# Performance work log

Measured on AMD Instinct MI355X. Metric: run time of the kernel, lower is better.

The kernel has to match this reference:

```python
import jax, jax.numpy as jnp
import numpy as np

B = 4096          # events per batch
K = 32            # neighbors stored per node
F = 64            # feat_dim = time_dim = e_feat_dim
H = 128           # hidden_dim = e_feat_dim + time_dim
DIN = 2 * F       # GRU input: [edge_emb | time_emb]
N_NODES = 500_000
N_EDGES = 1_000_000


def setup_inputs() -> dict:
    key = jax.random.key(0)
    ks = jax.random.split(key, 20)
    inp = {}
    inp["src_ids"] = jax.random.randint(ks[0], (B,), 0, N_NODES)
    inp["tgt_ids"] = jax.random.randint(ks[1], (B,), 0, N_NODES)
    inp["bad_ids"] = jax.random.randint(ks[2], (B,), 0, N_NODES)
    inp["cut_time"] = jax.random.uniform(ks[3], (B,)) * 1e4 + 1e4
    inp["ngh_id"] = jax.random.randint(ks[4], (3 * B, K), 0, N_NODES)
    inp["e_idx"] = jax.random.randint(ks[5], (3 * B, K), 0, N_EDGES)
    inp["ngh_ts"] = jax.random.uniform(ks[6], (3 * B, K)) * 1e4
    inp["hidden_store"] = jax.random.normal(ks[7], (3 * B, K, H)) * 0.1
    # frozen raw feature tables (padding row 0 zeroed like padding_idx=0)
    n_feat = jax.random.normal(ks[8], (N_NODES, F)) * 0.1
    inp["n_feat"] = n_feat.at[0].set(0.0)
    e_feat = jax.random.normal(ks[9], (N_EDGES, F)) * 0.1
    inp["e_feat"] = e_feat.at[0].set(0.0)
    # TimeEncode params
    inp["basis_freq"] = jnp.asarray(1.0 / 10 ** np.linspace(0, 9, F), jnp.float32)
    inp["phase"] = jnp.zeros((F,), jnp.float32)
    # GRUCell params (torch layout: [3H, in], gate order r,z,n)
    s = 1.0 / np.sqrt(H)
    inp["W_ih"] = jax.random.uniform(ks[10], (3 * H, DIN), minval=-s, maxval=s)
    inp["W_hh"] = jax.random.uniform(ks[11], (3 * H, H), minval=-s, maxval=s)
    inp["b_ih"] = jax.random.uniform(ks[12], (3 * H,), minval=-s, maxval=s)
    inp["b_hh"] = jax.random.uniform(ks[13], (3 * H,), minval=-s, maxval=s)
    # readout projection (stand-in for GAT output to feat_dim)
    inp["W_out"] = jax.random.normal(ks[14], (F, F + H)) * (1.0 / np.sqrt(F + H))
    inp["b_out"] = jnp.zeros((F,), jnp.float32)
    # MergeLayer (non_linear=True): fc1 [F, 2F], fc2 [1, F]
    inp["fc1_w"] = jax.random.normal(ks[15], (F, 2 * F)) * (1.0 / np.sqrt(2 * F))
    inp["fc1_b"] = jnp.zeros((F,), jnp.float32)
    inp["fc2_w"] = jax.random.normal(ks[16], (1, F)) * (1.0 / np.sqrt(F))
    inp["fc2_b"] = jnp.zeros((1,), jnp.float32)
    return inp


def _gru_cell(x, h, W_ih, W_hh, b_ih, b_hh):
    gx = x @ W_ih.T + b_ih          # [N, 3H]
    gh = h @ W_hh.T + b_hh
    xr, xz, xn = jnp.split(gx, 3, axis=-1)
    hr, hz, hn = jnp.split(gh, 3, axis=-1)
    r = jax.nn.sigmoid(xr + hr)
    z = jax.nn.sigmoid(xz + hz)
    n = jnp.tanh(xn + r * hn)
    return (1.0 - z) * n + z * h


def reference(src_ids, tgt_ids, bad_ids, cut_time, ngh_id, e_idx, ngh_ts,
              hidden_store, n_feat, e_feat, basis_freq, phase,
              W_ih, W_hh, b_ih, b_hh, W_out, b_out,
              fc1_w, fc1_b, fc2_w, fc2_b):
    ids = jnp.concatenate([src_ids, tgt_ids, bad_ids], 0)      # [3B]
    node_raw = n_feat[ids]                                     # [3B, F] gather
    e_emb = e_feat[e_idx]                                      # [3B, K, F] gather
    # cosine time encoding of time delta since neighbor event
    ct = jnp.tile(cut_time, 3)                                 # [3B]
    dt = ct[:, None] - ngh_ts                                  # [3B, K]
    ts_emb = jnp.cos(dt[..., None] * basis_freq + phase)       # [3B, K, F]
    # one GRUCell step per stored neighbor
    x = jnp.concatenate([e_emb, ts_emb], -1).reshape(-1, DIN)  # [3B*K, 2F]
    h = hidden_store.reshape(-1, H)
    h_new = _gru_cell(x, h, W_ih, W_hh, b_ih, b_hh).reshape(3 * B, K, H)
    # masked mean over valid neighbors (ngh_id 0 = padding)
    mask = (ngh_id != 0).astype(h_new.dtype)[..., None]        # [3B, K, 1]
    agg = (h_new * mask).sum(1) / jnp.maximum(mask.sum(1), 1.0)  # [3B, H]
    # readout to feat_dim
    emb = jax.nn.relu(jnp.concatenate([node_raw, agg], -1) @ W_out.T + b_out)
    src_e, tgt_e, bad_e = emb[:B], emb[B:2 * B], emb[2 * B:]
    def merge(x1, x2):
        hcat = jax.nn.relu(jnp.concatenate([x1, x2], -1) @ fc1_w.T + fc1_b)
        return hcat @ fc2_w.T + fc2_b                          # [B, 1]
    pos = merge(src_e, tgt_e)
    neg = merge(src_e, bad_e)
    return jnp.concatenate([pos, neg], -1)                     # [B, 2]
```

## Files before the change

kernel.cpp:

```cpp
#include <hip/hip_runtime.h>
#include <hip/hip_bf16.h>

#define B_SZ   4096

typedef short bf16x8 __attribute__((ext_vector_type(8)));
typedef float f32x4  __attribute__((ext_vector_type(4)));

__device__ __forceinline__ short f2bf(float f) {
    __hip_bfloat16 h = __float2bfloat16(f);
    return *reinterpret_cast<short*>(&h);
}
__device__ __forceinline__ float bf2f(unsigned int u16) {
    unsigned int x = u16 << 16;
    float f;
    __builtin_memcpy(&f, &x, 4);
    return f;
}
__device__ __forceinline__ float fsig(float x) {
    return __builtin_amdgcn_rcpf(1.0f + __expf(-x));
}
__device__ __forceinline__ float ftanhf(float x) {
    return 1.0f - 2.0f * __builtin_amdgcn_rcpf(__expf(2.0f * x) + 1.0f);
}
__device__ __forceinline__ int swz(int row, int cbyte) {
    return row * 512 + (cbyte ^ ((row & 7) << 4));
}

__global__ void prep_kernel(const float* __restrict__ wih, const float* __restrict__ whh,
                            short* __restrict__ wfrag) {
    int idx = blockIdx.x * 256 + threadIdx.x;
    int i   = idx & 7;
    int kh  = (idx >> 3) & 3;
    int j   = (idx >> 5) & 127;
    int gks = idx >> 12;
    int g   = gks >> 3, ks = gks & 7;
    int k   = ks * 32 + kh * 8 + i;
    int r   = g * 128 + j;
    float v = (k < 128) ? wih[r * 128 + k] : whh[r * 128 + (k - 128)];
    wfrag[idx] = f2bf(v);
}

__global__ __launch_bounds__(512, 4) void gru_agg_kernel(
    const int*   __restrict__ ngh_id,
    const int*   __restrict__ e_idx,
    const float* __restrict__ ngh_ts,
    const float* __restrict__ hidden_store,
    const float* __restrict__ e_feat,
    const float* __restrict__ basis_freq,
    const float* __restrict__ phase,
    const float* __restrict__ cut_time,
    const short* __restrict__ wfrag,
    const float* __restrict__ b_ih,
    const float* __restrict__ b_hh,
    float*       __restrict__ agg)
{
    __shared__ __align__(16) char sT[64 * 512];
    __shared__ float sMask[64];
    __shared__ float sInv[2];

    const int bid  = blockIdx.x;
    const int tid  = threadIdx.x;
    const int lane = tid & 63;
    const int wv   = tid >> 6;

    if (wv < 2) {
        const int row  = lane;
        const int flat = bid * 64 + row;
        const int e    = e_idx[flat];
        const float4* src = reinterpret_cast<const float4*>(e_feat + (size_t)e * 64 + wv * 32);
        float v[32];
        #pragma unroll
        for (int t = 0; t < 8; ++t) *reinterpret_cast<float4*>(&v[t * 4]) = src[t];
        union { bf16x8 w[4]; short s[32]; } u;
        #pragma unroll
        for (int i = 0; i < 32; ++i) u.s[i] = f2bf(v[i]);
        const int cb = wv * 64;
        #pragma unroll
        for (int t = 0; t < 4; ++t)
            *reinterpret_cast<bf16x8*>(&sT[swz(row, cb + t * 16)]) = u.w[t];
    } else if (wv < 4) {
        const int row  = lane;
        const int flat = bid * 64 + row;
        if (wv == 2) {
            const int nid = ngh_id[flat];
            sMask[row] = (nid != 0) ? 1.0f : 0.0f;
            unsigned long long mb = __ballot(nid != 0);
            if (lane == 0) {
                int c0n = __popcll(mb & 0xFFFFFFFFull);
                int c1n = __popcll(mb >> 32);
                sInv[0] = 1.0f / (float)(c0n > 1 ? c0n : 1);
                sInv[1] = 1.0f / (float)(c1n > 1 ? c1n : 1);
            }
        }
        const int rnode = bid * 2 + (row >> 5);
        const float dt  = cut_time[rnode & (B_SZ - 1)] - ngh_ts[flat];
        const int f0 = (wv - 2) * 32;
        float v[32];
        #pragma unroll
        for (int i = 0; i < 32; ++i)
            v[i] = __cosf(dt * basis_freq[f0 + i] + phase[f0 + i]);
        union { bf16x8 w[4]; short s[32]; } u;
        #pragma unroll
        for (int i = 0; i < 32; ++i) u.s[i] = f2bf(v[i]);
        const int cb = 128 + f0 * 2;
        #pragma unroll
        for (int t = 0; t < 4; ++t)
            *reinterpret_cast<bf16x8*>(&sT[swz(row, cb + t * 16)]) = u.w[t];
    } else {
        const int hw   = wv - 4;
        const int row  = hw * 16 + (lane >> 2);
        const int flat = bid * 64 + row;
        const int c0   = (lane & 3) * 32;
        const float4* src = reinterpret_cast<const float4*>(hidden_store + (size_t)flat * 128 + c0);
        float v[32];
        #pragma unroll
        for (int t = 0; t < 8; ++t) *reinterpret_cast<float4*>(&v[t * 4]) = src[t];
        union { bf16x8 w[4]; short s[32]; } u;
        #pragma unroll
        for (int i = 0; i < 32; ++i) u.s[i] = f2bf(v[i]);
        const int cb = 256 + c0 * 2;
        #pragma unroll
        for (int t = 0; t < 4; ++t)
            *reinterpret_cast<bf16x8*>(&sT[swz(row, cb + t * 16)]) = u.w[t];
    }
    __syncthreads();

    const int l15 = lane & 15;
    const int kh  = lane >> 4;
    const int jc  = (wv << 4) + l15;

    f32x4 ar[4], az[4], axn[4], ahn[4];
    #pragma unroll
    for (int mf = 0; mf < 4; ++mf) {
        ar[mf]  = (f32x4){0.f, 0.f, 0.f, 0.f};
        az[mf]  = (f32x4){0.f, 0.f, 0.f, 0.f};
        axn[mf] = (f32x4){0.f, 0.f, 0.f, 0.f};
        ahn[mf] = (f32x4){0.f, 0.f, 0.f, 0.f};
    }

    #pragma unroll
    for (int ks = 0; ks < 8; ++ks) {
        bf16x8 a[4];
        #pragma unroll
        for (int mf = 0; mf < 4; ++mf)
            a[mf] = *reinterpret_cast<const bf16x8*>(&sT[swz(mf * 16 + l15, ks * 64 + kh * 16)]);
        bf16x8 br = *reinterpret_cast<const bf16x8*>(wfrag + (((((0 * 8 + ks) * 128 + jc) << 2) + kh) << 3));
        bf16x8 bz = *reinterpret_cast<const bf16x8*>(wfrag + (((((1 * 8 + ks) * 128 + jc) << 2) + kh) << 3));
        bf16x8 bn = *reinterpret_cast<const bf16x8*>(wfrag + (((((2 * 8 + ks) * 128 + jc) << 2) + kh) << 3));
        #pragma unroll
        for (int mf = 0; mf < 4; ++mf)
            ar[mf] = __builtin_amdgcn_mfma_f32_16x16x32_bf16(a[mf], br, ar[mf], 0, 0, 0);
        #pragma unroll
        for (int mf = 0; mf < 4; ++mf)
            az[mf] = __builtin_amdgcn_mfma_f32_16x16x32_bf16(a[mf], bz, az[mf], 0, 0, 0);
        if (ks < 4) {
            #pragma unroll
            for (int mf = 0; mf < 4; ++mf)
                axn[mf] = __builtin_amdgcn_mfma_f32_16x16x32_bf16(a[mf], bn, axn[mf], 0, 0, 0);
        } else {
            #pragma unroll
            for (int mf = 0; mf < 4; ++mf)
                ahn[mf] = __builtin_amdgcn_mfma_f32_16x16x32_bf16(a[mf], bn, ahn[mf], 0, 0, 0);
        }
    }

    const float brz = b_ih[jc] + b_hh[jc];
    const float bzz = b_ih[128 + jc] + b_hh[128 + jc];
    const float bin = b_ih[256 + jc];
    const float bhn = b_hh[256 + jc];

    float s0 = 0.f, s1 = 0.f;
    #pragma unroll
    for (int mf = 0; mf < 4; ++mf) {
        #pragma unroll
        for (int i = 0; i < 4; ++i) {
            const int row = mf * 16 + kh * 4 + i;
            const float rr = fsig(ar[mf][i] + brz);
            const float zz = fsig(az[mf][i] + bzz);
            const float nn = ftanhf(axn[mf][i] + bin + rr * (ahn[mf][i] + bhn));
            const float hc = bf2f(*reinterpret_cast<const unsigned short*>(&sT[swz(row, 256 + jc * 2)]));
            const float hv = ((1.0f - zz) * nn + zz * hc) * sMask[row];
            if (mf < 2) s0 += hv; else s1 += hv;
        }
    }
    s0 += __shfl_xor(s0, 16, 64);
    s0 += __shfl_xor(s0, 32, 64);
    s1 += __shfl_xor(s1, 16, 64);
    s1 += __shfl_xor(s1, 32, 64);
    if (lane < 16) {
        agg[(bid * 2 + 0) * 128 + jc] = s0 * sInv[0];
        agg[(bid * 2 + 1) * 128 + jc] = s1 * sInv[1];
    }
}

__global__ __launch_bounds__(256) void emb_kernel(
    const int*   __restrict__ src_ids, const int* __restrict__ tgt_ids,
    const int*   __restrict__ bad_ids, const float* __restrict__ n_feat,
    const float* __restrict__ W_out,   const float* __restrict__ b_out,
    const float* __restrict__ agg,     float* __restrict__ emb)
{
    __shared__ float sv[16][192];
    const int base = blockIdx.x * 16;
    const int j  = threadIdx.x & 63;
    const int ng = threadIdx.x >> 6;
    #pragma unroll
    for (int n0 = 0; n0 < 4; ++n0) {
        const int n = ng * 4 + n0;
        const int node = base + n;
        int id;
        if (node < B_SZ)          id = src_ids[node];
        else if (node < 2 * B_SZ) id = tgt_ids[node - B_SZ];
        else                      id = bad_ids[node - 2 * B_SZ];
        sv[n][j]       = n_feat[(size_t)id * 64 + j];
        sv[n][64 + j]  = agg[(size_t)node * 128 + j];
        sv[n][128 + j] = agg[(size_t)node * 128 + 64 + j];
    }
    __syncthreads();
    float acc[4];
    const float bj = b_out[j];
    #pragma unroll
    for (int n0 = 0; n0 < 4; ++n0) acc[n0] = bj;
    const float4* wr = reinterpret_cast<const float4*>(W_out + j * 192);
    #pragma unroll 4
    for (int c = 0; c < 48; ++c) {
        float4 w = wr[c];
        #pragma unroll
        for (int n0 = 0; n0 < 4; ++n0) {
            const float* s = &sv[ng * 4 + n0][c * 4];
            acc[n0] += w.x * s[0] + w.y * s[1] + w.z * s[2] + w.w * s[3];
        }
    }
    #pragma unroll
    for (int n0 = 0; n0 < 4; ++n0)
        emb[(size_t)(base + ng * 4 + n0) * 64 + j] = fmaxf(acc[n0], 0.0f);
}

__global__ __launch_bounds__(256) void merge_kernel(
    const float* __restrict__ emb,  const float* __restrict__ fc1_w,
    const float* __restrict__ fc1_b, const float* __restrict__ fc2_w,
    const float* __restrict__ fc2_b, float* __restrict__ out)
{
    __shared__ float se[16][192];
    const int base = blockIdx.x * 16;
    const int j  = threadIdx.x & 63;
    const int ng = threadIdx.x >> 6;
    #pragma unroll
    for (int p0 = 0; p0 < 4; ++p0) {
        const int p = ng * 4 + p0;
        const int i = base + p;
        se[p][j]       = emb[(size_t)i * 64 + j];
        se[p][64 + j]  = emb[(size_t)(B_SZ + i) * 64 + j];
        se[p][128 + j] = emb[(size_t)(2 * B_SZ + i) * 64 + j];
    }
    __syncthreads();
    const float4* w1 = reinterpret_cast<const float4*>(fc1_w + j * 128);
    float sp[4] = {0, 0, 0, 0}, tp[4] = {0, 0, 0, 0}, bp[4] = {0, 0, 0, 0};
    #pragma unroll 4
    for (int c = 0; c < 16; ++c) {
        float4 wa = w1[c];
        float4 wb = w1[16 + c];
        #pragma unroll
        for (int p0 = 0; p0 < 4; ++p0) {
            const float* s = se[ng * 4 + p0];
            const float* sa = &s[c * 4];
            sp[p0] += wa.x * sa[0] + wa.y * sa[1] + wa.z * sa[2] + wa.w * sa[3];
            const float* st = &s[64 + c * 4];
            tp[p0] += wb.x * st[0] + wb.y * st[1] + wb.z * st[2] + wb.w * st[3];
            const float* sb = &s[128 + c * 4];
            bp[p0] += wb.x * sb[0] + wb.y * sb[1] + wb.z * sb[2] + wb.w * sb[3];
        }
    }
    const float b1 = fc1_b[j];
    const float w2 = fc2_w[j];
    #pragma unroll
    for (int p0 = 0; p0 < 4; ++p0) {
        float p = fmaxf(b1 + sp[p0] + tp[p0], 0.f) * w2;
        float n = fmaxf(b1 + sp[p0] + bp[p0], 0.f) * w2;
        #pragma unroll
        for (int m = 32; m >= 1; m >>= 1) {
            p += __shfl_xor(p, m, 64);
            n += __shfl_xor(n, m, 64);
        }
        if (j == 0) {
            const int i = base + ng * 4 + p0;
            out[2 * i]     = p + fc2_b[0];
            out[2 * i + 1] = n + fc2_b[0];
        }
    }
}

extern "C" void kernel_launch(void* const* d_in, const int* in_sizes, int n_in,
                              void* d_out, int out_size, void* d_ws, size_t ws_size,
                              hipStream_t stream) {
    const int*   src_ids  = (const int*)  d_in[0];
    const int*   tgt_ids  = (const int*)  d_in[1];
    const int*   bad_ids  = (const int*)  d_in[2];
    const float* cut_time = (const float*)d_in[3];
    const int*   ngh_id   = (const int*)  d_in[4];
    const int*   e_idx    = (const int*)  d_in[5];
    const float* ngh_ts   = (const float*)d_in[6];
    const float* hidden   = (const float*)d_in[7];
    const float* n_feat   = (const float*)d_in[8];
    const float* e_feat   = (const float*)d_in[9];
    const float* basis    = (const float*)d_in[10];
    const float* phase    = (const float*)d_in[11];
    const float* W_ih     = (const float*)d_in[12];
    const float* W_hh     = (const float*)d_in[13];
    const float* b_ih     = (const float*)d_in[14];
    const float* b_hh     = (const float*)d_in[15];
    const float* W_out    = (const float*)d_in[16];
    const float* b_out    = (const float*)d_in[17];
    const float* fc1_w    = (const float*)d_in[18];
    const float* fc1_b    = (const float*)d_in[19];
    const float* fc2_w    = (const float*)d_in[20];
    const float* fc2_b    = (const float*)d_in[21];

    char* ws = (char*)d_ws;
    short* wfrag = (short*)(ws);
    float* agg   = (float*)(ws + 196608);
    float* emb   = (float*)(ws + 196608 + 6291456);
    float* out   = (float*)d_out;

    hipLaunchKernelGGL(prep_kernel, dim3(384), dim3(256), 0, stream, W_ih, W_hh, wfrag);
    hipLaunchKernelGGL(gru_agg_kernel, dim3(6144), dim3(512), 0, stream,
                       ngh_id, e_idx, ngh_ts, hidden, e_feat, basis, phase, cut_time,
                       wfrag, b_ih, b_hh, agg);
    hipLaunchKernelGGL(emb_kernel, dim3(768), dim3(256), 0, stream,
                       src_ids, tgt_ids, bad_ids, n_feat, W_out, b_out, agg, emb);
    hipLaunchKernelGGL(merge_kernel, dim3(256), dim3(256), 0, stream,
                       emb, fc1_w, fc1_b, fc2_w, fc2_b, out);
}
```

Measured before the change: 181.7 us.

## Process one node per GRU block to halve tile size and raise occupancy

```diff
diff --git a/kernel.cpp b/kernel.cpp
--- a/kernel.cpp
+++ b/kernel.cpp
@@ -24,6 +24,13 @@
 }
 __device__ __forceinline__ int swz(int row, int cbyte) {
     return row * 512 + (cbyte ^ ((row & 7) << 4));
+}
+__device__ __forceinline__ void pack16(const float* v, bf16x8* out) {
+    union { short s[16]; bf16x8 w[2]; } u;
+    #pragma unroll
+    for (int i = 0; i < 16; ++i) u.s[i] = f2bf(v[i]);
+    out[0] = u.w[0];
+    out[1] = u.w[1];
 }
 
 __global__ void prep_kernel(const float* __restrict__ wih, const float* __restrict__ whh,
@@ -40,7 +47,7 @@
     wfrag[idx] = f2bf(v);
 }
 
-__global__ __launch_bounds__(512, 4) void gru_agg_kernel(
+__global__ __launch_bounds__(512, 6) void gru_agg_kernel(
     const int*   __restrict__ ngh_id,
     const int*   __restrict__ e_idx,
     const float* __restrict__ ngh_ts,
@@ -54,74 +61,56 @@
     const float* __restrict__ b_hh,
     float*       __restrict__ agg)
 {
-    __shared__ __align__(16) char sT[64 * 512];
-    __shared__ float sMask[64];
-    __shared__ float sInv[2];
+    __shared__ __align__(16) char sT[32 * 512];
+    __shared__ float sMask[32];
+    __shared__ float sInv;
 
     const int bid  = blockIdx.x;
     const int tid  = threadIdx.x;
     const int lane = tid & 63;
     const int wv   = tid >> 6;
 
-    if (wv < 2) {
-        const int row  = lane;
-        const int flat = bid * 64 + row;
-        const int e    = e_idx[flat];
-        const float4* src = reinterpret_cast<const float4*>(e_feat + (size_t)e * 64 + wv * 32);
-        float v[32];
-        #pragma unroll
-        for (int t = 0; t < 8; ++t) *reinterpret_cast<float4*>(&v[t * 4]) = src[t];
-        union { bf16x8 w[4]; short s[32]; } u;
-        #pragma unroll
-        for (int i = 0; i < 32; ++i) u.s[i] = f2bf(v[i]);
-        const int cb = wv * 64;
-        #pragma unroll
-        for (int t = 0; t < 4; ++t)
-            *reinterpret_cast<bf16x8*>(&sT[swz(row, cb + t * 16)]) = u.w[t];
-    } else if (wv < 4) {
-        const int row  = lane;
-        const int flat = bid * 64 + row;
-        if (wv == 2) {
-            const int nid = ngh_id[flat];
-            sMask[row] = (nid != 0) ? 1.0f : 0.0f;
-            unsigned long long mb = __ballot(nid != 0);
-            if (lane == 0) {
-                int c0n = __popcll(mb & 0xFFFFFFFFull);
-                int c1n = __popcll(mb >> 32);
-                sInv[0] = 1.0f / (float)(c0n > 1 ? c0n : 1);
-                sInv[1] = 1.0f / (float)(c1n > 1 ? c1n : 1);
+    {
+        const int row  = lane & 31;
+        const int h    = lane >> 5;
+        const int flat = bid * 32 + row;
+        float v[16];
+        int cb;
+
+        if (wv < 2) {
+            if (wv == 0) {
+                const int nid = ngh_id[flat];
+                unsigned long long mb = __ballot(nid != 0);
+                if (lane < 32) sMask[row] = (nid != 0) ? 1.0f : 0.0f;
+                if (lane == 0) {
+                    int c = __popcll(mb & 0xFFFFFFFFull);
+                    sInv = 1.0f / (float)(c > 1 ? c : 1);
+                }
             }
-        }
-        const int rnode = bid * 2 + (row >> 5);
-        const float dt  = cut_time[rnode & (B_SZ - 1)] - ngh_ts[flat];
-        const int f0 = (wv - 2) * 32;
-        float v[32];
-        #pragma unroll
-        for (int i = 0; i < 32; ++i)
-            v[i] = __cosf(dt * basis_freq[f0 + i] + phase[f0 + i]);
-        union { bf16x8 w[4]; short s[32]; } u;
-        #pragma unroll
-        for (int i = 0; i < 32; ++i) u.s[i] = f2bf(v[i]);
-        const int cb = 128 + f0 * 2;
-        #pragma unroll
-        for (int t = 0; t < 4; ++t)
-            *reinterpret_cast<bf16x8*>(&sT[swz(row, cb + t * 16)]) = u.w[t];
-    } else {
-        const int hw   = wv - 4;
-        const int row  = hw * 16 + (lane >> 2);
-        const int flat = bid * 64 + row;
-        const int c0   = (lane & 3) * 32;
-        const float4* src = reinterpret_cast<const float4*>(hidden_store + (size_t)flat * 128 + c0);
-        float v[32];
-        #pragma unroll
-        for (int t = 0; t < 8; ++t) *reinterpret_cast<float4*>(&v[t * 4]) = src[t];
-        union { bf16x8 w[4]; short s[32]; } u;
-        #pragma unroll
-        for (int i = 0; i < 32; ++i) u.s[i] = f2bf(v[i]);
-        const int cb = 256 + c0 * 2;
-        #pragma unroll
-        for (int t = 0; t < 4; ++t)
-            *reinterpret_cast<bf16x8*>(&sT[swz(row, cb + t * 16)]) = u.w[t];
+            const int c0 = wv * 32 + h * 16;
+            const int e  = e_idx[flat];
+            const float4* src = reinterpret_cast<const float4*>(e_feat + (size_t)e * 64 + c0);
+            #pragma unroll
+            for (int t = 0; t < 4; ++t) *reinterpret_cast<float4*>(&v[t * 4]) = src[t];
+            cb = c0 * 2;
+        } else if (wv < 4) {
+            const float dt = cut_time[bid & (B_SZ - 1)] - ngh_ts[flat];
+            const int f0 = (wv - 2) * 32 + h * 16;
+            #pragma unroll
+            for (int i = 0; i < 16; ++i)
+                v[i] = __cosf(dt * basis_freq[f0 + i] + phase[f0 + i]);
+            cb = 128 + f0 * 2;
+        } else {
+            const int c0 = (wv - 4) * 32 + h * 16;
+            const float4* src = reinterpret_cast<const float4*>(hidden_store + (size_t)flat * 128 + c0);
+            #pragma unroll
+            for (int t = 0; t < 4; ++t) *reinterpret_cast<float4*>(&v[t * 4]) = src[t];
+            cb = 256 + c0 * 2;
+        }
+        bf16x8 w[2];
+        pack16(v, w);
+        *reinterpret_cast<bf16x8*>(&sT[swz(row, cb)])      = w[0];
+        *reinterpret_cast<bf16x8*>(&sT[swz(row, cb + 16)]) = w[1];
     }
     __syncthreads();
 
@@ -129,9 +118,9 @@
     const int kh  = lane >> 4;
     const int jc  = (wv << 4) + l15;
 
-    f32x4 ar[4], az[4], axn[4], ahn[4];
-    #pragma unroll
-    for (int mf = 0; mf < 4; ++mf) {
+    f32x4 ar[2], az[2], axn[2], ahn[2];
+    #pragma unroll
+    for (int mf = 0; mf < 2; ++mf) {
         ar[mf]  = (f32x4){0.f, 0.f, 0.f, 0.f};
         az[mf]  = (f32x4){0.f, 0.f, 0.f, 0.f};
         axn[mf] = (f32x4){0.f, 0.f, 0.f, 0.f};
@@ -140,26 +129,26 @@
 
     #pragma unroll
     for (int ks = 0; ks < 8; ++ks) {
-        bf16x8 a[4];
-        #pragma unroll
-        for (int mf = 0; mf < 4; ++mf)
+        bf16x8 a[2];
+        #pragma unroll
+        for (int mf = 0; mf < 2; ++mf)
             a[mf] = *reinterpret_cast<const bf16x8*>(&sT[swz(mf * 16 + l15, ks * 64 + kh * 16)]);
         bf16x8 br = *reinterpret_cast<const bf16x8*>(wfrag + (((((0 * 8 + ks) * 128 + jc) << 2) + kh) << 3));
         bf16x8 bz = *reinterpret_cast<const bf16x8*>(wfrag + (((((1 * 8 + ks) * 128 + jc) << 2) + kh) << 3));
         bf16x8 bn = *reinterpret_cast<const bf16x8*>(wfrag + (((((2 * 8 + ks) * 128 + jc) << 2) + kh) << 3));
         #pragma unroll
-        for (int mf = 0; mf < 4; ++mf)
+        for (int mf = 0; mf < 2; ++mf)
             ar[mf] = __builtin_amdgcn_mfma_f32_16x16x32_bf16(a[mf], br, ar[mf], 0, 0, 0);
         #pragma unroll
-        for (int mf = 0; mf < 4; ++mf)
+        for (int mf = 0; mf < 2; ++mf)
             az[mf] = __builtin_amdgcn_mfma_f32_16x16x32_bf16(a[mf], bz, az[mf], 0, 0, 0);
         if (ks < 4) {
             #pragma unroll
-            for (int mf = 0; mf < 4; ++mf)
+            for (int mf = 0; mf < 2; ++mf)
                 axn[mf] = __builtin_amdgcn_mfma_f32_16x16x32_bf16(a[mf], bn, axn[mf], 0, 0, 0);
         } else {
             #pragma unroll
-            for (int mf = 0; mf < 4; ++mf)
+            for (int mf = 0; mf < 2; ++mf)
                 ahn[mf] = __builtin_amdgcn_mfma_f32_16x16x32_bf16(a[mf], bn, ahn[mf], 0, 0, 0);
         }
     }
@@ -169,9 +158,9 @@
     const float bin = b_ih[256 + jc];
     const float bhn = b_hh[256 + jc];
 
-    float s0 = 0.f, s1 = 0.f;
-    #pragma unroll
-    for (int mf = 0; mf < 4; ++mf) {
+    float s = 0.f;
+    #pragma unroll
+    for (int mf = 0; mf < 2; ++mf) {
         #pragma unroll
         for (int i = 0; i < 4; ++i) {
             const int row = mf * 16 + kh * 4 + i;
@@ -179,18 +168,13 @@
             const float zz = fsig(az[mf][i] + bzz);
             const float nn = ftanhf(axn[mf][i] + bin + rr * (ahn[mf][i] + bhn));
             const float hc = bf2f(*reinterpret_cast<const unsigned short*>(&sT[swz(row, 256 + jc * 2)]));
-            const float hv = ((1.0f - zz) * nn + zz * hc) * sMask[row];
-            if (mf < 2) s0 += hv; else s1 += hv;
-        }
-    }
-    s0 += __shfl_xor(s0, 16, 64);
-    s0 += __shfl_xor(s0, 32, 64);
-    s1 += __shfl_xor(s1, 16, 64);
-    s1 += __shfl_xor(s1, 32, 64);
-    if (lane < 16) {
-        agg[(bid * 2 + 0) * 128 + jc] = s0 * sInv[0];
-        agg[(bid * 2 + 1) * 128 + jc] = s1 * sInv[1];
-    }
+            s += ((1.0f - zz) * nn + zz * hc) * sMask[row];
+        }
+    }
+    s += __shfl_xor(s, 16, 64);
+    s += __shfl_xor(s, 32, 64);
+    if (lane < 16)
+        agg[(size_t)bid * 128 + jc] = s * sInv;
 }
 
 __global__ __launch_bounds__(256) void emb_kernel(
@@ -322,7 +306,7 @@
     float* out   = (float*)d_out;
 
     hipLaunchKernelGGL(prep_kernel, dim3(384), dim3(256), 0, stream, W_ih, W_hh, wfrag);
-    hipLaunchKernelGGL(gru_agg_kernel, dim3(6144), dim3(512), 0, stream,
+    hipLaunchKernelGGL(gru_agg_kernel, dim3(12288), dim3(512), 0, stream,
                        ngh_id, e_idx, ngh_ts, hidden, e_feat, basis, phase, cut_time,
                        wfrag, b_ih, b_hh, agg);
     hipLaunchKernelGGL(emb_kernel, dim3(768), dim3(256), 0, stream,
```

After: 229.3 us. 1.26x slower.

## Split GRU gate MFMA phases and pack r/z gates to bf16 to cut registers

Applied to the files above, without the earlier changes.

```diff
diff --git a/kernel.cpp b/kernel.cpp
--- a/kernel.cpp
+++ b/kernel.cpp
@@ -15,6 +15,11 @@
     float f;
     __builtin_memcpy(&f, &x, 4);
     return f;
+}
+__device__ __forceinline__ unsigned int pk2(float a, float b) {
+    unsigned int lo = (unsigned short)f2bf(a);
+    unsigned int hi = (unsigned short)f2bf(b);
+    return lo | (hi << 16);
 }
 __device__ __forceinline__ float fsig(float x) {
     return __builtin_amdgcn_rcpf(1.0f + __expf(-x));
@@ -40,7 +45,7 @@
     wfrag[idx] = f2bf(v);
 }
 
-__global__ __launch_bounds__(512, 4) void gru_agg_kernel(
+__global__ __launch_bounds__(512, 6) void gru_agg_kernel(
     const int*   __restrict__ ngh_id,
     const int*   __restrict__ e_idx,
     const float* __restrict__ ngh_ts,
@@ -129,15 +134,12 @@
     const int kh  = lane >> 4;
     const int jc  = (wv << 4) + l15;
 
-    f32x4 ar[4], az[4], axn[4], ahn[4];
+    f32x4 ar[4], az[4];
     #pragma unroll
     for (int mf = 0; mf < 4; ++mf) {
-        ar[mf]  = (f32x4){0.f, 0.f, 0.f, 0.f};
-        az[mf]  = (f32x4){0.f, 0.f, 0.f, 0.f};
-        axn[mf] = (f32x4){0.f, 0.f, 0.f, 0.f};
-        ahn[mf] = (f32x4){0.f, 0.f, 0.f, 0.f};
-    }
-
+        ar[mf] = (f32x4){0.f, 0.f, 0.f, 0.f};
+        az[mf] = (f32x4){0.f, 0.f, 0.f, 0.f};
+    }
     #pragma unroll
     for (int ks = 0; ks < 8; ++ks) {
         bf16x8 a[4];
@@ -146,13 +148,43 @@
             a[mf] = *reinterpret_cast<const bf16x8*>(&sT[swz(mf * 16 + l15, ks * 64 + kh * 16)]);
         bf16x8 br = *reinterpret_cast<const bf16x8*>(wfrag + (((((0 * 8 + ks) * 128 + jc) << 2) + kh) << 3));
         bf16x8 bz = *reinterpret_cast<const bf16x8*>(wfrag + (((((1 * 8 + ks) * 128 + jc) << 2) + kh) << 3));
-        bf16x8 bn = *reinterpret_cast<const bf16x8*>(wfrag + (((((2 * 8 + ks) * 128 + jc) << 2) + kh) << 3));
         #pragma unroll
         for (int mf = 0; mf < 4; ++mf)
             ar[mf] = __builtin_amdgcn_mfma_f32_16x16x32_bf16(a[mf], br, ar[mf], 0, 0, 0);
         #pragma unroll
         for (int mf = 0; mf < 4; ++mf)
             az[mf] = __builtin_amdgcn_mfma_f32_16x16x32_bf16(a[mf], bz, az[mf], 0, 0, 0);
+    }
+
+    const float brz = b_ih[jc] + b_hh[jc];
+    const float bzz = b_ih[128 + jc] + b_hh[128 + jc];
+    unsigned int rrpk[8], zzpk[8];
+    #pragma unroll
+    for (int mf = 0; mf < 4; ++mf) {
+        #pragma unroll
+        for (int p = 0; p < 2; ++p) {
+            float r0 = fsig(ar[mf][2 * p]     + brz);
+            float r1 = fsig(ar[mf][2 * p + 1] + brz);
+            float z0 = fsig(az[mf][2 * p]     + bzz);
+            float z1 = fsig(az[mf][2 * p + 1] + bzz);
+            rrpk[mf * 2 + p] = pk2(r0, r1);
+            zzpk[mf * 2 + p] = pk2(z0, z1);
+        }
+    }
+
+    f32x4 axn[4], ahn[4];
+    #pragma unroll
+    for (int mf = 0; mf < 4; ++mf) {
+        axn[mf] = (f32x4){0.f, 0.f, 0.f, 0.f};
+        ahn[mf] = (f32x4){0.f, 0.f, 0.f, 0.f};
+    }
+    #pragma unroll
+    for (int ks = 0; ks < 8; ++ks) {
+        bf16x8 a[4];
+        #pragma unroll
+        for (int mf = 0; mf < 4; ++mf)
+            a[mf] = *reinterpret_cast<const bf16x8*>(&sT[swz(mf * 16 + l15, ks * 64 + kh * 16)]);
+        bf16x8 bn = *reinterpret_cast<const bf16x8*>(wfrag + (((((2 * 8 + ks) * 128 + jc) << 2) + kh) << 3));
         if (ks < 4) {
             #pragma unroll
             for (int mf = 0; mf < 4; ++mf)
@@ -164,8 +196,6 @@
         }
     }
 
-    const float brz = b_ih[jc] + b_hh[jc];
-    const float bzz = b_ih[128 + jc] + b_hh[128 + jc];
     const float bin = b_ih[256 + jc];
     const float bhn = b_hh[256 + jc];
 
@@ -175,11 +205,13 @@
         #pragma unroll
         for (int i = 0; i < 4; ++i) {
             const int row = mf * 16 + kh * 4 + i;
-            const float rr = fsig(ar[mf][i] + brz);
-            const float zz = fsig(az[mf][i] + bzz);
-            const float nn = ftanhf(axn[mf][i] + bin + rr * (ahn[mf][i] + bhn));
-            const float hc = bf2f(*reinterpret_cast<const unsigned short*>(&sT[swz(row, 256 + jc * 2)]));
-            const float hv = ((1.0f - zz) * nn + zz * hc) * sMask[row];
+            unsigned int rp = rrpk[mf * 2 + (i >> 1)];
+            unsigned int zp = zzpk[mf * 2 + (i >> 1)];
+            float rr = bf2f((i & 1) ? (rp >> 16) : (rp & 0xffffu));
+            float zz = bf2f((i & 1) ? (zp >> 16) : (zp & 0xffffu));
+            float nn = ftanhf(axn[mf][i] + bin + rr * (ahn[mf][i] + bhn));
+            float hc = bf2f(*reinterpret_cast<const unsigned short*>(&sT[swz(row, 256 + jc * 2)]));
+            float hv = ((1.0f - zz) * nn + zz * hc) * sMask[row];
             if (mf < 2) s0 += hv; else s1 += hv;
         }
     }
```

Measured after the change: 318.4 us. 1.75x slower.

## Make GRU aggregation kernel persistent with async LDS prefetch of next tile

Applied to the files above, without the earlier changes.

```diff
diff --git a/kernel.cpp b/kernel.cpp
--- a/kernel.cpp
+++ b/kernel.cpp
@@ -2,8 +2,10 @@
 #include <hip/hip_bf16.h>
 
 #define B_SZ   4096
+#define NT     12
 
 typedef short bf16x8 __attribute__((ext_vector_type(8)));
+typedef short bf16x4 __attribute__((ext_vector_type(4)));
 typedef float f32x4  __attribute__((ext_vector_type(4)));
 
 __device__ __forceinline__ short f2bf(float f) {
@@ -24,6 +26,12 @@
 }
 __device__ __forceinline__ int swz(int row, int cbyte) {
     return row * 512 + (cbyte ^ ((row & 7) << 4));
+}
+__device__ __forceinline__ void gld16(const float* g, float* l) {
+    __builtin_amdgcn_global_load_lds(
+        (const __attribute__((address_space(1))) void*)g,
+        (__attribute__((address_space(3))) void*)l,
+        16, 0, 0);
 }
 
 __global__ void prep_kernel(const float* __restrict__ wih, const float* __restrict__ whh,
@@ -54,142 +62,181 @@
     const float* __restrict__ b_hh,
     float*       __restrict__ agg)
 {
-    __shared__ __align__(16) char sT[64 * 512];
-    __shared__ float sMask[64];
-    __shared__ float sInv[2];
-
-    const int bid  = blockIdx.x;
+    __shared__ float sE[4096];
+    __shared__ float sH8[8192];
+    __shared__ __align__(16) char sT[32768];
+
     const int tid  = threadIdx.x;
     const int lane = tid & 63;
     const int wv   = tid >> 6;
-
-    if (wv < 2) {
-        const int row  = lane;
-        const int flat = bid * 64 + row;
-        const int e    = e_idx[flat];
-        const float4* src = reinterpret_cast<const float4*>(e_feat + (size_t)e * 64 + wv * 32);
-        float v[32];
-        #pragma unroll
-        for (int t = 0; t < 8; ++t) *reinterpret_cast<float4*>(&v[t * 4]) = src[t];
-        union { bf16x8 w[4]; short s[32]; } u;
-        #pragma unroll
-        for (int i = 0; i < 32; ++i) u.s[i] = f2bf(v[i]);
-        const int cb = wv * 64;
-        #pragma unroll
-        for (int t = 0; t < 4; ++t)
-            *reinterpret_cast<bf16x8*>(&sT[swz(row, cb + t * 16)]) = u.w[t];
-    } else if (wv < 4) {
-        const int row  = lane;
-        const int flat = bid * 64 + row;
-        if (wv == 2) {
-            const int nid = ngh_id[flat];
-            sMask[row] = (nid != 0) ? 1.0f : 0.0f;
-            unsigned long long mb = __ballot(nid != 0);
-            if (lane == 0) {
-                int c0n = __popcll(mb & 0xFFFFFFFFull);
-                int c1n = __popcll(mb >> 32);
-                sInv[0] = 1.0f / (float)(c0n > 1 ? c0n : 1);
-                sInv[1] = 1.0f / (float)(c1n > 1 ? c1n : 1);
-            }
-        }
-        const int rnode = bid * 2 + (row >> 5);
-        const float dt  = cut_time[rnode & (B_SZ - 1)] - ngh_ts[flat];
-        const int f0 = (wv - 2) * 32;
-        float v[32];
-        #pragma unroll
-        for (int i = 0; i < 32; ++i)
-            v[i] = __cosf(dt * basis_freq[f0 + i] + phase[f0 + i]);
-        union { bf16x8 w[4]; short s[32]; } u;
-        #pragma unroll
-        for (int i = 0; i < 32; ++i) u.s[i] = f2bf(v[i]);
-        const int cb = 128 + f0 * 2;
-        #pragma unroll
-        for (int t = 0; t < 4; ++t)
-            *reinterpret_cast<bf16x8*>(&sT[swz(row, cb + t * 16)]) = u.w[t];
-    } else {
-        const int hw   = wv - 4;
-        const int row  = hw * 16 + (lane >> 2);
-        const int flat = bid * 64 + row;
-        const int c0   = (lane & 3) * 32;
-        const float4* src = reinterpret_cast<const float4*>(hidden_store + (size_t)flat * 128 + c0);
-        float v[32];
-        #pragma unroll
-        for (int t = 0; t < 8; ++t) *reinterpret_cast<float4*>(&v[t * 4]) = src[t];
-        union { bf16x8 w[4]; short s[32]; } u;
-        #pragma unroll
-        for (int i = 0; i < 32; ++i) u.s[i] = f2bf(v[i]);
-        const int cb = 256 + c0 * 2;
-        #pragma unroll
-        for (int t = 0; t < 4; ++t)
-            *reinterpret_cast<bf16x8*>(&sT[swz(row, cb + t * 16)]) = u.w[t];
-    }
-    __syncthreads();
-
-    const int l15 = lane & 15;
-    const int kh  = lane >> 4;
-    const int jc  = (wv << 4) + l15;
-
-    f32x4 ar[4], az[4], axn[4], ahn[4];
-    #pragma unroll
-    for (int mf = 0; mf < 4; ++mf) {
-        ar[mf]  = (f32x4){0.f, 0.f, 0.f, 0.f};
-        az[mf]  = (f32x4){0.f, 0.f, 0.f, 0.f};
-        axn[mf] = (f32x4){0.f, 0.f, 0.f, 0.f};
-        ahn[mf] = (f32x4){0.f, 0.f, 0.f, 0.f};
-    }
-
-    #pragma unroll
-    for (int ks = 0; ks < 8; ++ks) {
-        bf16x8 a[4];
-        #pragma unroll
-        for (int mf = 0; mf < 4; ++mf)
-            a[mf] = *reinterpret_cast<const bf16x8*>(&sT[swz(mf * 16 + l15, ks * 64 + kh * 16)]);
-        bf16x8 br = *reinterpret_cast<const bf16x8*>(wfrag + (((((0 * 8 + ks) * 128 + jc) << 2) + kh) << 3));
-        bf16x8 bz = *reinterpret_cast<const bf16x8*>(wfrag + (((((1 * 8 + ks) * 128 + jc) << 2) + kh) << 3));
-        bf16x8 bn = *reinterpret_cast<const bf16x8*>(wfrag + (((((2 * 8 + ks) * 128 + jc) << 2) + kh) << 3));
-        #pragma unroll
-        for (int mf = 0; mf < 4; ++mf)
-            ar[mf] = __builtin_amdgcn_mfma_f32_16x16x32_bf16(a[mf], br, ar[mf], 0, 0, 0);
-        #pragma unroll
-        for (int mf = 0; mf < 4; ++mf)
-            az[mf] = __builtin_amdgcn_mfma_f32_16x16x32_bf16(a[mf], bz, az[mf], 0, 0, 0);
-        if (ks < 4) {
-            #pragma unroll
-            for (int mf = 0; mf < 4; ++mf)
-                axn[mf] = __builtin_amdgcn_mfma_f32_16x16x32_bf16(a[mf], bn, axn[mf], 0, 0, 0);
-        } else {
-            #pragma unroll
-            for (int mf = 0; mf < 4; ++mf)
-                ahn[mf] = __builtin_amdgcn_mfma_f32_16x16x32_bf16(a[mf], bn, ahn[mf], 0, 0, 0);
-        }
-    }
+    const int l15  = lane & 15;
+    const int kh   = lane >> 4;
+    const int jc   = (wv << 4) + l15;
+
+    const int tsrow = tid >> 3;
+    const int tscol = (tid & 7) * 8;
 
     const float brz = b_ih[jc] + b_hh[jc];
     const float bzz = b_ih[128 + jc] + b_hh[128 + jc];
     const float bin = b_ih[256 + jc];
     const float bhn = b_hh[256 + jc];
 
-    float s0 = 0.f, s1 = 0.f;
-    #pragma unroll
-    for (int mf = 0; mf < 4; ++mf) {
-        #pragma unroll
-        for (int i = 0; i < 4; ++i) {
-            const int row = mf * 16 + kh * 4 + i;
-            const float rr = fsig(ar[mf][i] + brz);
-            const float zz = fsig(az[mf][i] + bzz);
-            const float nn = ftanhf(axn[mf][i] + bin + rr * (ahn[mf][i] + bhn));
-            const float hc = bf2f(*reinterpret_cast<const unsigned short*>(&sT[swz(row, 256 + jc * 2)]));
-            const float hv = ((1.0f - zz) * nn + zz * hc) * sMask[row];
-            if (mf < 2) s0 += hv; else s1 += hv;
-        }
-    }
-    s0 += __shfl_xor(s0, 16, 64);
-    s0 += __shfl_xor(s0, 32, 64);
-    s1 += __shfl_xor(s1, 16, 64);
-    s1 += __shfl_xor(s1, 32, 64);
-    if (lane < 16) {
-        agg[(bid * 2 + 0) * 128 + jc] = s0 * sInv[0];
-        agg[(bid * 2 + 1) * 128 + jc] = s1 * sInv[1];
+    const int tile0 = blockIdx.x * NT;
+    const int erow  = wv * 8 + (lane >> 4);
+
+    float tsr  = ngh_ts[(size_t)tile0 * 64 + tsrow];
+    float ctr  = cut_time[(tile0 * 2 + (tsrow >> 5)) & (B_SZ - 1)];
+    int   ngid = ngh_id[(size_t)tile0 * 64 + lane];
+    int iA = e_idx[(size_t)tile0 * 64 + erow];
+    int iB = e_idx[(size_t)tile0 * 64 + erow + 4];
+    gld16(e_feat + (size_t)iA * 64 + l15 * 4, &sE[(wv * 2 + 0) * 256]);
+    gld16(e_feat + (size_t)iB * 64 + l15 * 4, &sE[(wv * 2 + 1) * 256]);
+    #pragma unroll
+    for (int k = 0; k < 4; ++k)
+        gld16(hidden_store + (size_t)(tile0 * 64 + wv * 8 + k * 2 + (lane >> 5)) * 128 + (lane & 31) * 4,
+              &sH8[(wv * 4 + k) * 256]);
+    int cA = e_idx[(size_t)(tile0 + 1) * 64 + erow];
+    int cB = e_idx[(size_t)(tile0 + 1) * 64 + erow + 4];
+
+    __syncthreads();
+
+    {
+        #pragma unroll
+        for (int j = 0; j < 2; ++j) {
+            float4 v = *reinterpret_cast<const float4*>(&sE[(wv * 2 + j) * 256 + lane * 4]);
+            int row = wv * 8 + j * 4 + (lane >> 4);
+            bf16x4 o = { f2bf(v.x), f2bf(v.y), f2bf(v.z), f2bf(v.w) };
+            *reinterpret_cast<bf16x4*>(&sT[swz(row, l15 * 8)]) = o;
+        }
+        #pragma unroll
+        for (int k = 0; k < 4; ++k) {
+            float4 v = *reinterpret_cast<const float4*>(&sH8[(wv * 4 + k) * 256 + lane * 4]);
+            int row = wv * 8 + k * 2 + (lane >> 5);
+            bf16x4 o = { f2bf(v.x), f2bf(v.y), f2bf(v.z), f2bf(v.w) };
+            *reinterpret_cast<bf16x4*>(&sT[swz(row, 256 + (lane & 31) * 8)]) = o;
+        }
+        const float dt = ctr - tsr;
+        union { short s[8]; bf16x8 w; } u;
+        #pragma unroll
+        for (int i = 0; i < 8; ++i)
+            u.s[i] = f2bf(__cosf(dt * basis_freq[tscol + i] + phase[tscol + i]));
+        *reinterpret_cast<bf16x8*>(&sT[swz(tsrow, 128 + (tid & 7) * 16)]) = u.w;
+    }
+    unsigned long long mb = __ballot(ngid != 0);
+    int c0n = __popcll(mb & 0xFFFFFFFFull);
+    int c1n = __popcll(mb >> 32);
+    float inv0 = 1.0f / (float)(c0n > 1 ? c0n : 1);
+    float inv1 = 1.0f / (float)(c1n > 1 ? c1n : 1);
+    __syncthreads();
+
+    #pragma unroll 1
+    for (int t = 0; t < NT; ++t) {
+        const int tt = tile0 + t;
+        float n_tsr = 0.f, n_ctr = 0.f;
+        int   n_ngid = 0;
+        if (t + 1 < NT) {
+            gld16(e_feat + (size_t)cA * 64 + l15 * 4, &sE[(wv * 2 + 0) * 256]);
+            gld16(e_feat + (size_t)cB * 64 + l15 * 4, &sE[(wv * 2 + 1) * 256]);
+            #pragma unroll
+            for (int k = 0; k < 4; ++k)
+                gld16(hidden_store + (size_t)((tt + 1) * 64 + wv * 8 + k * 2 + (lane >> 5)) * 128 + (lane & 31) * 4,
+                      &sH8[(wv * 4 + k) * 256]);
+            n_tsr  = ngh_ts[(size_t)(tt + 1) * 64 + tsrow];
+            n_ctr  = cut_time[((tt + 1) * 2 + (tsrow >> 5)) & (B_SZ - 1)];
+            n_ngid = ngh_id[(size_t)(tt + 1) * 64 + lane];
+            const int t2 = (t + 2 < NT) ? (tt + 2) : (tile0 + NT - 1);
+            cA = e_idx[(size_t)t2 * 64 + erow];
+            cB = e_idx[(size_t)t2 * 64 + erow + 4];
+        }
+
+        f32x4 ar[4], az[4], axn[4], ahn[4];
+        #pragma unroll
+        for (int mf = 0; mf < 4; ++mf) {
+            ar[mf]  = (f32x4){0.f, 0.f, 0.f, 0.f};
+            az[mf]  = (f32x4){0.f, 0.f, 0.f, 0.f};
+            axn[mf] = (f32x4){0.f, 0.f, 0.f, 0.f};
+            ahn[mf] = (f32x4){0.f, 0.f, 0.f, 0.f};
+        }
+        #pragma unroll
+        for (int ks = 0; ks < 8; ++ks) {
+            bf16x8 a[4];
+            #pragma unroll
+            for (int mf = 0; mf < 4; ++mf)
+                a[mf] = *reinterpret_cast<const bf16x8*>(&sT[swz(mf * 16 + l15, ks * 64 + kh * 16)]);
+            bf16x8 br = *reinterpret_cast<const bf16x8*>(wfrag + (((((0 * 8 + ks) * 128 + jc) << 2) + kh) << 3));
+            bf16x8 bz = *reinterpret_cast<const bf16x8*>(wfrag + (((((1 * 8 + ks) * 128 + jc) << 2) + kh) << 3));
+            bf16x8 bn = *reinterpret_cast<const bf16x8*>(wfrag + (((((2 * 8 + ks) * 128 + jc) << 2) + kh) << 3));
+            #pragma unroll
+            for (int mf = 0; mf < 4; ++mf)
+                ar[mf] = __builtin_amdgcn_mfma_f32_16x16x32_bf16(a[mf], br, ar[mf], 0, 0, 0);
+            #pragma unroll
+            for (int mf = 0; mf < 4; ++mf)
+                az[mf] = __builtin_amdgcn_mfma_f32_16x16x32_bf16(a[mf], bz, az[mf], 0, 0, 0);
+            if (ks < 4) {
+                #pragma unroll
+                for (int mf = 0; mf < 4; ++mf)
+                    axn[mf] = __builtin_amdgcn_mfma_f32_16x16x32_bf16(a[mf], bn, axn[mf], 0, 0, 0);
+            } else {
+                #pragma unroll
+                for (int mf = 0; mf < 4; ++mf)
+                    ahn[mf] = __builtin_amdgcn_mfma_f32_16x16x32_bf16(a[mf], bn, ahn[mf], 0, 0, 0);
+            }
+        }
+
+        float s0 = 0.f, s1 = 0.f;
+        #pragma unroll
+        for (int mf = 0; mf < 4; ++mf) {
+            #pragma unroll
+            for (int i = 0; i < 4; ++i) {
+                const int row = mf * 16 + kh * 4 + i;
+                const float rr = fsig(ar[mf][i] + brz);
+                const float zz = fsig(az[mf][i] + bzz);
+                const float nn = ftanhf(axn[mf][i] + bin + rr * (ahn[mf][i] + bhn));
+                const float hc = bf2f(*reinterpret_cast<const unsigned short*>(&sT[swz(row, 256 + jc * 2)]));
+                const float m  = (float)((mb >> row) & 1ull);
+                const float hv = ((1.0f - zz) * nn + zz * hc) * m;
+                if (mf < 2) s0 += hv; else s1 += hv;
+            }
+        }
+        s0 += __shfl_xor(s0, 16, 64);
+        s0 += __shfl_xor(s0, 32, 64);
+        s1 += __shfl_xor(s1, 16, 64);
+        s1 += __shfl_xor(s1, 32, 64);
+        if (lane < 16) {
+            agg[(size_t)(tt * 2 + 0) * 128 + jc] = s0 * inv0;
+            agg[(size_t)(tt * 2 + 1) * 128 + jc] = s1 * inv1;
+        }
+
+        if (t + 1 < NT) {
+            __syncthreads();
+            #pragma unroll
+            for (int j = 0; j < 2; ++j) {
+                float4 v = *reinterpret_cast<const float4*>(&sE[(wv * 2 + j) * 256 + lane * 4]);
+                int row = wv * 8 + j * 4 + (lane >> 4);
+                bf16x4 o = { f2bf(v.x), f2bf(v.y), f2bf(v.z), f2bf(v.w) };
+                *reinterpret_cast<bf16x4*>(&sT[swz(row, l15 * 8)]) = o;
+            }
+            #pragma unroll
+            for (int k = 0; k < 4; ++k) {
+                float4 v = *reinterpret_cast<const float4*>(&sH8[(wv * 4 + k) * 256 + lane * 4]);
+                int row = wv * 8 + k * 2 + (lane >> 5);
+                bf16x4 o = { f2bf(v.x), f2bf(v.y), f2bf(v.z), f2bf(v.w) };
+                *reinterpret_cast<bf16x4*>(&sT[swz(row, 256 + (lane & 31) * 8)]) = o;
+            }
+            const float dt = n_ctr - n_tsr;
+            union { short s[8]; bf16x8 w; } u;
+            #pragma unroll
+            for (int i = 0; i < 8; ++i)
+                u.s[i] = f2bf(__cosf(dt * basis_freq[tscol + i] + phase[tscol + i]));
+            *reinterpret_cast<bf16x8*>(&sT[swz(tsrow, 128 + (tid & 7) * 16)]) = u.w;
+
+            mb  = __ballot(n_ngid != 0);
+            c0n = __popcll(mb & 0xFFFFFFFFull);
+            c1n = __popcll(mb >> 32);
+            inv0 = 1.0f / (float)(c0n > 1 ? c0n : 1);
+            inv1 = 1.0f / (float)(c1n > 1 ? c1n : 1);
+            __syncthreads();
+        }
     }
 }
 
@@ -322,7 +369,7 @@
     float* out   = (float*)d_out;
 
     hipLaunchKernelGGL(prep_kernel, dim3(384), dim3(256), 0, stream, W_ih, W_hh, wfrag);
-    hipLaunchKernelGGL(gru_agg_kernel, dim3(6144), dim3(512), 0, stream,
+    hipLaunchKernelGGL(gru_agg_kernel, dim3(512), dim3(512), 0, stream,
                        ngh_id, e_idx, ngh_ts, hidden, e_feat, basis, phase, cut_time,
                        wfrag, b_ih, b_hh, agg);
     hipLaunchKernelGGL(emb_kernel, dim3(768), dim3(256), 0, stream,
```

After: 465.3 us. 2.56x slower.
